# Kernel optimization log

Hardware: AMD Instinct MI355X
Metric: run time of the kernel (lower is better)

Reference implementation:

```python
import jax, jax.numpy as jnp
import numpy as np

B, T, IN, HID, LAT = 256, 512, 128, 64, 16

def _mk_lstm(key, in_dim, h_dim, scale):
    k1, k2, k3, k4 = jax.random.split(key, 4)
    return (jax.random.normal(k1, (4 * h_dim, in_dim), jnp.float32) * scale,
            jax.random.normal(k2, (4 * h_dim, h_dim), jnp.float32) * scale,
            jax.random.normal(k3, (4 * h_dim,), jnp.float32) * scale,
            jax.random.normal(k4, (4 * h_dim,), jnp.float32) * scale)

def setup_inputs() -> dict:
    key = jax.random.key(0)
    ks = jax.random.split(key, 5)
    x = jax.random.normal(ks[0], (B, T, IN), jnp.float32)
    out = {"x": x}
    dims = [(IN, HID, "e1"), (HID, LAT, "e2"), (LAT, HID, "d1"), (HID, IN, "d2")]
    for k, (di, dh, nm) in zip(ks[1:], dims):
        scale = 1.0 / np.sqrt(dh)  # pytorch LSTM init range ~ 1/sqrt(hidden)
        Wih, Whh, bih, bhh = _mk_lstm(k, di, dh, scale)
        out[f"Wih_{nm}"], out[f"Whh_{nm}"], out[f"bih_{nm}"], out[f"bhh_{nm}"] = Wih, Whh, bih, bhh
    return out

def lstm(x, Wih, Whh, bih, bhh):
    # x: [B,T,I]; gates ordered i,f,g,o as in torch.nn.LSTM
    H = Whh.shape[1]
    xg = jnp.einsum('bti,gi->btg', x, Wih) + bih + bhh  # [B,T,4H]
    def step(carry, xt):
        h, c = carry
        g = xt + h @ Whh.T
        i, f, gg, o = jnp.split(g, 4, axis=-1)
        c = jax.nn.sigmoid(f) * c + jax.nn.sigmoid(i) * jnp.tanh(gg)
        h = jax.nn.sigmoid(o) * jnp.tanh(c)
        return (h, c), h
    b = x.shape[0]
    h0 = jnp.zeros((b, H), x.dtype)
    _, hs = jax.lax.scan(step, (h0, h0), jnp.swapaxes(xg, 0, 1))
    return jnp.swapaxes(hs, 0, 1)  # [B,T,H]

def reference(x, Wih_e1, Whh_e1, bih_e1, bhh_e1, Wih_e2, Whh_e2, bih_e2, bhh_e2,
              Wih_d1, Whh_d1, bih_d1, bhh_d1, Wih_d2, Whh_d2, bih_d2, bhh_d2):
    # dropout layers are identity at inference
    out = jax.nn.relu(lstm(x, Wih_e1, Whh_e1, bih_e1, bhh_e1))
    out = jax.nn.relu(lstm(out, Wih_e2, Whh_e2, bih_e2, bhh_e2))
    latent = out[:, -1, :]                                  # [B,LAT]
    dec_in = jnp.broadcast_to(latent[:, None, :], (x.shape[0], x.shape[1], latent.shape[-1]))
    out = jax.nn.relu(lstm(dec_in, Wih_d1, Whh_d1, bih_d1, bhh_d1))
    return lstm(out, Wih_d2, Whh_d2, bih_d2, bhh_d2)        # [B,T,IN]
```

## Files before the change

kernel.cpp:

```cpp
#include <hip/hip_runtime.h>


#define BB 256
#define TT 512

typedef _Float16 half2v __attribute__((ext_vector_type(2)));

static __device__ __forceinline__ float dot2(half2v a, half2v b, float c){
  return __builtin_amdgcn_fdot2(a,b,c,false);
}
template<int CTRL>
static __device__ __forceinline__ float qb(float v){
  return __int_as_float(__builtin_amdgcn_update_dpp(0, __float_as_int(v), CTRL, 0xF, 0xF, true));
}
static __device__ __forceinline__ float qsum1(float v){ return v + qb<0xB1>(v); }
static __device__ __forceinline__ float qsum2(float v){ return v + qb<0x4E>(v); }
static __device__ __forceinline__ float hsum8(float v){
  v = qsum1(v); v = qsum2(v); return v + qb<0x141>(v);
}
static __device__ __forceinline__ float rcp_(float v){ return __builtin_amdgcn_rcpf(v); }
static __device__ __forceinline__ unsigned packh2(float lo, float hi){
  half2v p; p.x=(_Float16)lo; p.y=(_Float16)hi;
  return __builtin_bit_cast(unsigned, p);
}
static __device__ __forceinline__ half2v ash2(unsigned u){ return __builtin_bit_cast(half2v,u); }
static __device__ __forceinline__ half2v mkh2(float lo, float hi){
  half2v p; p.x=(_Float16)lo; p.y=(_Float16)hi; return p;
}

static __device__ __forceinline__ float lstm_update(int q, float a0, float a1,
                                                    float a2, float a3, float& c){
  float mine = a0;
  mine = (q==1) ? a1 : mine;
  mine = (q==2) ? a2 : mine;
  mine = (q==3) ? a3 : mine;
  const bool isg = (q==2);
  const float arg = isg ? (mine+mine) : mine;
  const float s   = rcp_(1.0f + __expf(-arg));
  const float act = isg ? (s+s-1.0f) : s;
  const float bi = qb<0x00>(act);
  const float bf = qb<0x55>(act);
  const float bg = qb<0xAA>(act);
  const float bo = qb<0xFF>(act);
  c = bf*c + bi*bg;
  const float s2 = rcp_(1.0f + __expf(-(c+c)));
  return bo*(s2+s2-1.0f);
}

__global__ void __launch_bounds__(512, 2) k_fused(
    const float* __restrict__ x,
    const float* __restrict__ WihE1, const float* __restrict__ WhhE1,
    const float* __restrict__ bihE1, const float* __restrict__ bhhE1,
    const float* __restrict__ WihE2, const float* __restrict__ WhhE2,
    const float* __restrict__ bihE2, const float* __restrict__ bhhE2,
    const float* __restrict__ WihD1, const float* __restrict__ WhhD1,
    const float* __restrict__ bihD1, const float* __restrict__ bhhD1,
    const float* __restrict__ WihD2, const float* __restrict__ WhhD2,
    const float* __restrict__ bihD2, const float* __restrict__ bhhD2,
    float* __restrict__ out)
{
  const int b = blockIdx.x, tid = threadIdx.x;

  __shared__ unsigned wD1L[8*1024];
  __shared__ unsigned vhE [2*96];
  __shared__ unsigned e2op[2*48];
  __shared__ unsigned dop [2*96];
  __shared__ unsigned vhD1[2*32];
  __shared__ float4   bD2L[128];
  __shared__ float4   pD1L[64];
  __shared__ float    latF[16];

  {
    const int o = tid & 7, j = tid >> 3;
    half2v w1[4][12];
    float bias1[4];
#pragma unroll
    for (int g=0; g<4; ++g){
      const int row = g*64 + j;
      bias1[g] = (o==0) ? (bihE1[row]+bhhE1[row]) : 0.0f;
#pragma unroll
      for (int m=0;m<12;++m){
        const int k0 = 24*o + 2*m;
        const float lo = (k0   < 128)? WihE1[row*128+k0]   : WhhE1[row*64 + (k0-128)];
        const float hi = (k0+1 < 128)? WihE1[row*128+k0+1] : WhhE1[row*64 + (k0+1-128)];
        w1[g][m] = mkh2(lo,hi);
      }
    }
    const bool e2act = (tid >= 64 && tid < 128);
    const int q2 = tid & 3, j2 = (tid - 64) >> 2;
    half2v w2[4][12];
    float bias2[4] = {0.f,0.f,0.f,0.f};
    if (e2act){
#pragma unroll
      for (int g=0; g<4; ++g){
        const int row = g*16 + j2;
        bias2[g] = (q2==0) ? (bihE2[row]+bhhE2[row]) : 0.0f;
#pragma unroll
        for (int m=0;m<12;++m){
          const int k0 = 24*q2 + 2*m;
          float lo = 0.0f, hi = 0.0f;
          if (k0 < 64)        lo = WihE2[row*64+k0];
          else if (k0 < 80)   lo = WhhE2[row*16 + (k0-64)];
          if (k0+1 < 64)      hi = WihE2[row*64+k0+1];
          else if (k0+1 < 80) hi = WhhE2[row*16 + (k0+1-64)];
          w2[g][m] = mkh2(lo,hi);
        }
      }
    }
    const bool xact = (tid < 64);
    const float* xrow = x + (size_t)b * (TT*128);
    float2 xa, xb;
    if (xact){
      float2 v0 = *(const float2*)(xrow + 2*tid);
      vhE[tid] = packh2(v0.x, v0.y);
      xa = *(const float2*)(xrow + 128 + 2*tid);
      xb = *(const float2*)(xrow + 256 + 2*tid);
    }
    if (tid >= 128 && tid < 160) vhE[64 + (tid-128)] = 0u;
    if (tid >= 160 && tid < 256) e2op[tid-160] = 0u;
    float c1 = 0.0f, c2 = 0.0f;
    __syncthreads();

#define XSTAGE(T, NXT) do{ if (xact){                                          \
      vhE[(NXT)*96 + tid] = packh2(xa.x, xa.y);                                \
      xa = xb;                                                                 \
      const int t3_ = ((T)+3 < TT) ? ((T)+3) : (TT-1);                         \
      xb = *(const float2*)(xrow + (size_t)t3_*128 + 2*tid);                   \
    } }while(0)

#define E1STEP(T, CUR) do{                                                     \
      float a0=bias1[0], a1=bias1[1], a2=bias1[2], a3=bias1[3];                \
      const uint4* vp = (const uint4*)(vhE + (CUR)*96 + o*12);                 \
      _Pragma("unroll")                                                        \
      for (int r=0;r<3;++r){                                                   \
        const uint4 u = vp[r];                                                 \
        const half2v o0=ash2(u.x), o1=ash2(u.y), o2=ash2(u.z), o3=ash2(u.w);   \
        a0=dot2(w1[0][4*r+0],o0,a0); a1=dot2(w1[1][4*r+0],o0,a1);              \
        a2=dot2(w1[2][4*r+0],o0,a2); a3=dot2(w1[3][4*r+0],o0,a3);              \
        a0=dot2(w1[0][4*r+1],o1,a0); a1=dot2(w1[1][4*r+1],o1,a1);              \
        a2=dot2(w1[2][4*r+1],o1,a2); a3=dot2(w1[3][4*r+1],o1,a3);              \
        a0=dot2(w1[0][4*r+2],o2,a0); a1=dot2(w1[1][4*r+2],o2,a1);              \
        a2=dot2(w1[2][4*r+2],o2,a2); a3=dot2(w1[3][4*r+2],o2,a3);              \
        a0=dot2(w1[0][4*r+3],o3,a0); a1=dot2(w1[1][4*r+3],o3,a1);              \
        a2=dot2(w1[2][4*r+3],o3,a2); a3=dot2(w1[3][4*r+3],o3,a3);              \
      }                                                                        \
      a0=hsum8(a0); a1=hsum8(a1); a2=hsum8(a2); a3=hsum8(a3);                  \
      const float h = lstm_update(o & 3, a0, a1, a2, a3, c1);                  \
      if (o == 0){                                                             \
        ((_Float16*)(vhE + ((CUR)^1)*96))[128 + j] = (_Float16)h;              \
        ((_Float16*)(e2op + (CUR)*48))[j]          = (_Float16)fmaxf(h, 0.0f); \
      }                                                                        \
    }while(0)

#define E2STEP(T2, CP) do{ if (e2act){                                         \
      float a0=bias2[0], a1=bias2[1], a2=bias2[2], a3=bias2[3];                \
      const uint4* vp = (const uint4*)(e2op + (CP)*48 + q2*12);                \
      _Pragma("unroll")                                                        \
      for (int r=0;r<3;++r){                                                   \
        const uint4 u = vp[r];                                                 \
        const half2v o0=ash2(u.x), o1=ash2(u.y), o2=ash2(u.z), o3=ash2(u.w);   \
        a0=dot2(w2[0][4*r+0],o0,a0); a1=dot2(w2[1][4*r+0],o0,a1);              \
        a2=dot2(w2[2][4*r+0],o0,a2); a3=dot2(w2[3][4*r+0],o0,a3);              \
        a0=dot2(w2[0][4*r+1],o1,a0); a1=dot2(w2[1][4*r+1],o1,a1);              \
        a2=dot2(w2[2][4*r+1],o1,a2); a3=dot2(w2[3][4*r+1],o1,a3);              \
        a0=dot2(w2[0][4*r+2],o2,a0); a1=dot2(w2[1][4*r+2],o2,a1);              \
        a2=dot2(w2[2][4*r+2],o2,a2); a3=dot2(w2[3][4*r+2],o2,a3);              \
        a0=dot2(w2[0][4*r+3],o3,a0); a1=dot2(w2[1][4*r+3],o3,a1);              \
        a2=dot2(w2[2][4*r+3],o3,a2); a3=dot2(w2[3][4*r+3],o3,a3);              \
      }                                                                        \
      a0=qsum2(qsum1(a0)); a1=qsum2(qsum1(a1));                                \
      a2=qsum2(qsum1(a2)); a3=qsum2(qsum1(a3));                                \
      const float h = lstm_update(q2, a0, a1, a2, a3, c2);                     \
      if (q2 == 0){                                                            \
        ((_Float16*)(e2op + ((CP)^1)*48))[64 + j2] = (_Float16)h;              \
        if ((T2) == TT-1) latF[j2] = fmaxf(h, 0.0f);                           \
      }                                                                        \
    } }while(0)

    XSTAGE(0, 1); E1STEP(0, 0);
    __syncthreads();
    for (int t = 1; t <= TT-3; t += 2){
      XSTAGE(t, 0);   E1STEP(t, 1);   E2STEP(t-1, 0);
      __syncthreads();
      XSTAGE(t+1, 1); E1STEP(t+1, 0); E2STEP(t, 1);
      __syncthreads();
    }
    XSTAGE(TT-1, 0); E1STEP(TT-1, 1); E2STEP(TT-2, 0);
    __syncthreads();
    E2STEP(TT-1, 1);
    __syncthreads();
#undef XSTAGE
#undef E1STEP
#undef E2STEP
  }
  __syncthreads();
  asm volatile("" ::: "memory");

  {
#pragma unroll
    for (int i=0;i<16;++i){
      const int idx = i*512 + tid;
      const int r = idx >> 10, rem = idx & 1023, l = rem >> 2, d = rem & 3;
      const int jd_ = l >> 2, qd_ = l & 3, g = r >> 1, m = ((r & 1) << 2) + d;
      const int row = g*64 + jd_, k0 = qd_*16 + 2*m;
      wD1L[idx] = packh2(WhhD1[row*64+k0], WhhD1[row*64+k0+1]);
    }
    if (tid < 128){
      float4 bb;
      bb.x = bihD2[0*128+tid] + bhhD2[0*128+tid];
      bb.y = bihD2[1*128+tid] + bhhD2[1*128+tid];
      bb.z = bihD2[2*128+tid] + bhhD2[2*128+tid];
      bb.w = bihD2[3*128+tid] + bhhD2[3*128+tid];
      bD2L[tid] = bb;
    }
    if (tid < 64){
      float4 pp;
#pragma unroll
      for (int g=0; g<4; ++g){
        const int row = g*64 + tid;
        float a = bihD1[row] + bhhD1[row];
#pragma unroll
        for (int i=0;i<16;++i) a = fmaf(WihD1[row*16+i], latF[i], a);
        (&pp.x)[g] = a;
      }
      pD1L[tid] = pp;
    }

    const int qd = tid & 3, jd = tid >> 2;
    half2v wD2[4][24];
#pragma unroll
    for (int g=0; g<4; ++g){
      const int row = g*128 + jd;
#pragma unroll
      for (int m=0;m<24;++m){
        const int k0 = 48*qd + 2*m;
        const float lo = (k0   < 64)? WihD2[row*64+k0]   : WhhD2[row*128+(k0-64)];
        const float hi = (k0+1 < 64)? WihD2[row*64+k0+1] : WhhD2[row*128+(k0+1-64)];
        wD2[g][m] = mkh2(lo,hi);
      }
    }
    const bool d1act = (tid < 256);
    if (tid < 64)                dop[32 + tid] = 0u;
    if (tid >= 64 && tid < 96)   vhD1[tid-64] = 0u;
    float cd1 = 0.0f, cd2 = 0.0f;
    float* orow = out + (size_t)b * (TT*128);
    __syncthreads();

#define D2STEP(T2, C2P) do{                                                    \
      float a0=0.f, a1=0.f, a2=0.f, a3=0.f;                                    \
      const uint4* vp = (const uint4*)(dop + (C2P)*96 + qd*24);                \
      _Pragma("unroll")                                                        \
      for (int r=0;r<6;++r){                                                   \
        const uint4 u = vp[r];                                                 \
        const half2v o0=ash2(u.x),o1=ash2(u.y),o2=ash2(u.z),o3=ash2(u.w);      \
        a0=dot2(wD2[0][4*r+0],o0,a0); a1=dot2(wD2[1][4*r+0],o0,a1);            \
        a2=dot2(wD2[2][4*r+0],o0,a2); a3=dot2(wD2[3][4*r+0],o0,a3);            \
        a0=dot2(wD2[0][4*r+1],o1,a0); a1=dot2(wD2[1][4*r+1],o1,a1);            \
        a2=dot2(wD2[2][4*r+1],o1,a2); a3=dot2(wD2[3][4*r+1],o1,a3);            \
        a0=dot2(wD2[0][4*r+2],o2,a0); a1=dot2(wD2[1][4*r+2],o2,a1);            \
        a2=dot2(wD2[2][4*r+2],o2,a2); a3=dot2(wD2[3][4*r+2],o2,a3);            \
        a0=dot2(wD2[0][4*r+3],o3,a0); a1=dot2(wD2[1][4*r+3],o3,a1);            \
        a2=dot2(wD2[2][4*r+3],o3,a2); a3=dot2(wD2[3][4*r+3],o3,a3);            \
      }                                                                        \
      a0=qsum2(qsum1(a0)); a1=qsum2(qsum1(a1));                                \
      a2=qsum2(qsum1(a2)); a3=qsum2(qsum1(a3));                                \
      const float4 bb = bD2L[jd];                                              \
      a0 += bb.x; a1 += bb.y; a2 += bb.z; a3 += bb.w;                          \
      const float h = lstm_update(qd, a0, a1, a2, a3, cd2);                    \
      if (qd==0){                                                              \
        ((_Float16*)(dop + ((C2P)^1)*96))[64 + jd] = (_Float16)h;              \
        orow[(size_t)(T2)*128 + jd] = h;                                       \
      }                                                                        \
    }while(0)

#define D1STEP(T, CUR) do{ if (d1act){                                         \
      const uint4* ov = (const uint4*)(vhD1 + (CUR)*32 + qd*8);                \
      const uint4 o01 = ov[0], o23 = ov[1];                                    \
      float a0=0.f, a1=0.f, a2=0.f, a3=0.f;                                    \
      {                                                                        \
        const uint4 wA = *(const uint4*)(wD1L + 0*1024 + tid*4);               \
        const uint4 wB = *(const uint4*)(wD1L + 1*1024 + tid*4);               \
        a0=dot2(ash2(wA.x),ash2(o01.x),a0); a0=dot2(ash2(wA.y),ash2(o01.y),a0);\
        a0=dot2(ash2(wA.z),ash2(o01.z),a0); a0=dot2(ash2(wA.w),ash2(o01.w),a0);\
        a0=dot2(ash2(wB.x),ash2(o23.x),a0); a0=dot2(ash2(wB.y),ash2(o23.y),a0);\
        a0=dot2(ash2(wB.z),ash2(o23.z),a0); a0=dot2(ash2(wB.w),ash2(o23.w),a0);\
      }                                                                        \
      {                                                                        \
        const uint4 wA = *(const uint4*)(wD1L + 2*1024 + tid*4);               \
        const uint4 wB = *(const uint4*)(wD1L + 3*1024 + tid*4);               \
        a1=dot2(ash2(wA.x),ash2(o01.x),a1); a1=dot2(ash2(wA.y),ash2(o01.y),a1);\
        a1=dot2(ash2(wA.z),ash2(o01.z),a1); a1=dot2(ash2(wA.w),ash2(o01.w),a1);\
        a1=dot2(ash2(wB.x),ash2(o23.x),a1); a1=dot2(ash2(wB.y),ash2(o23.y),a1);\
        a1=dot2(ash2(wB.z),ash2(o23.z),a1); a1=dot2(ash2(wB.w),ash2(o23.w),a1);\
      }                                                                        \
      {                                                                        \
        const uint4 wA = *(const uint4*)(wD1L + 4*1024 + tid*4);               \
        const uint4 wB = *(const uint4*)(wD1L + 5*1024 + tid*4);               \
        a2=dot2(ash2(wA.x),ash2(o01.x),a2); a2=dot2(ash2(wA.y),ash2(o01.y),a2);\
        a2=dot2(ash2(wA.z),ash2(o01.z),a2); a2=dot2(ash2(wA.w),ash2(o01.w),a2);\
        a2=dot2(ash2(wB.x),ash2(o23.x),a2); a2=dot2(ash2(wB.y),ash2(o23.y),a2);\
        a2=dot2(ash2(wB.z),ash2(o23.z),a2); a2=dot2(ash2(wB.w),ash2(o23.w),a2);\
      }                                                                        \
      {                                                                        \
        const uint4 wA = *(const uint4*)(wD1L + 6*1024 + tid*4);               \
        const uint4 wB = *(const uint4*)(wD1L + 7*1024 + tid*4);               \
        a3=dot2(ash2(wA.x),ash2(o01.x),a3); a3=dot2(ash2(wA.y),ash2(o01.y),a3);\
        a3=dot2(ash2(wA.z),ash2(o01.z),a3); a3=dot2(ash2(wA.w),ash2(o01.w),a3);\
        a3=dot2(ash2(wB.x),ash2(o23.x),a3); a3=dot2(ash2(wB.y),ash2(o23.y),a3);\
        a3=dot2(ash2(wB.z),ash2(o23.z),a3); a3=dot2(ash2(wB.w),ash2(o23.w),a3);\
      }                                                                        \
      a0=qsum2(qsum1(a0)); a1=qsum2(qsum1(a1));                                \
      a2=qsum2(qsum1(a2)); a3=qsum2(qsum1(a3));                                \
      const float4 pj = pD1L[jd];                                              \
      a0 += pj.x; a1 += pj.y; a2 += pj.z; a3 += pj.w;                          \
      const float h = lstm_update(qd, a0, a1, a2, a3, cd1);                    \
      if (qd==0){                                                              \
        ((_Float16*)(vhD1 + ((CUR)^1)*32))[jd] = (_Float16)h;                  \
        ((_Float16*)(dop + (CUR)*96))[jd]      = (_Float16)fmaxf(h,0.0f);      \
      }                                                                        \
    } }while(0)

    D1STEP(0, 0);
    __syncthreads();
    for (int t = 1; t <= TT-3; t += 2){
      D2STEP(t-1, 0); D1STEP(t, 1);
      __syncthreads();
      D2STEP(t, 1);   D1STEP(t+1, 0);
      __syncthreads();
    }
    D2STEP(TT-2, 0); D1STEP(TT-1, 1);
    __syncthreads();
    D2STEP(TT-1, 1);
#undef D2STEP
#undef D1STEP
  }
}

extern "C" void kernel_launch(void* const* d_in, const int* in_sizes, int n_in,
                              void* d_out, int out_size, void* d_ws, size_t ws_size,
                              hipStream_t stream) {
  const float* x      = (const float*)d_in[0];
  const float* WihE1  = (const float*)d_in[1];
  const float* WhhE1  = (const float*)d_in[2];
  const float* bihE1  = (const float*)d_in[3];
  const float* bhhE1  = (const float*)d_in[4];
  const float* WihE2  = (const float*)d_in[5];
  const float* WhhE2  = (const float*)d_in[6];
  const float* bihE2  = (const float*)d_in[7];
  const float* bhhE2  = (const float*)d_in[8];
  const float* WihD1  = (const float*)d_in[9];
  const float* WhhD1  = (const float*)d_in[10];
  const float* bihD1  = (const float*)d_in[11];
  const float* bhhD1  = (const float*)d_in[12];
  const float* WihD2  = (const float*)d_in[13];
  const float* WhhD2  = (const float*)d_in[14];
  const float* bihD2  = (const float*)d_in[15];
  const float* bhhD2  = (const float*)d_in[16];
  float* out = (float*)d_out;

  k_fused<<<BB, 512, 0, stream>>>(x,
      WihE1, WhhE1, bihE1, bhhE1,
      WihE2, WhhE2, bihE2, bhhE2,
      WihD1, WhhD1, bihD1, bhhD1,
      WihD2, WhhD2, bihD2, bhhD2,
      out);
}
```

Before: 775.4 us.

## Remap encoder warps: 4-lane E1 groups, E2 weights in LDS, separate x-stage warp

Encoder layer 1 now uses 4 lanes per hidden unit with 24 half2 weights per gate in registers, instead of 8 lanes with 12. This shortens the cross-lane reduction from three DPP steps to two. E2 weights move from registers into a shared-memory table read each step, and E1, E2 and the x staging are given separate waves (threads 0-255, 256-319, 320-383). The intent is to cut reduction latency on the serial critical path and avoid divergence inside one wave. In exchange, E1 register pressure roughly doubles, which risks spills under the 512-thread, 2-block launch bounds, and E2 pays extra LDS reads every step.

```diff
diff --git a/kernel.cpp b/kernel.cpp
--- a/kernel.cpp
+++ b/kernel.cpp
@@ -15,9 +15,6 @@
 }
 static __device__ __forceinline__ float qsum1(float v){ return v + qb<0xB1>(v); }
 static __device__ __forceinline__ float qsum2(float v){ return v + qb<0x4E>(v); }
-static __device__ __forceinline__ float hsum8(float v){
-  v = qsum1(v); v = qsum2(v); return v + qb<0x141>(v);
-}
 static __device__ __forceinline__ float rcp_(float v){ return __builtin_amdgcn_rcpf(v); }
 static __device__ __forceinline__ unsigned packh2(float lo, float hi){
   half2v p; p.x=(_Float16)lo; p.y=(_Float16)hi;
@@ -62,6 +59,7 @@
   const int b = blockIdx.x, tid = threadIdx.x;
 
   __shared__ unsigned wD1L[8*1024];
+  __shared__ unsigned e2wL[12*256];
   __shared__ unsigned vhE [2*96];
   __shared__ unsigned e2op[2*48];
   __shared__ unsigned dop [2*96];
@@ -71,50 +69,56 @@
   __shared__ float    latF[16];
 
   {
-    const int o = tid & 7, j = tid >> 3;
-    half2v w1[4][12];
-    float bias1[4];
-#pragma unroll
-    for (int g=0; g<4; ++g){
-      const int row = g*64 + j;
-      bias1[g] = (o==0) ? (bihE1[row]+bhhE1[row]) : 0.0f;
-#pragma unroll
-      for (int m=0;m<12;++m){
-        const int k0 = 24*o + 2*m;
-        const float lo = (k0   < 128)? WihE1[row*128+k0]   : WhhE1[row*64 + (k0-128)];
-        const float hi = (k0+1 < 128)? WihE1[row*128+k0+1] : WhhE1[row*64 + (k0+1-128)];
-        w1[g][m] = mkh2(lo,hi);
-      }
-    }
-    const bool e2act = (tid >= 64 && tid < 128);
-    const int q2 = tid & 3, j2 = (tid - 64) >> 2;
-    half2v w2[4][12];
-    float bias2[4] = {0.f,0.f,0.f,0.f};
-    if (e2act){
+#pragma unroll
+    for (int i=0;i<6;++i){
+      const int idx = i*512 + tid;
+      const int r_ = idx >> 8, rem = idx & 255, l = rem >> 2, d = rem & 3;
+      const int g = r_/3, rr = r_ - 3*g, m = rr*4 + d;
+      const int q2l = l & 3, j2l = l >> 2;
+      const int row = g*16 + j2l, k0 = q2l*24 + 2*m;
+      float lo = 0.0f, hi = 0.0f;
+      if (k0 < 64)        lo = WihE2[row*64+k0];
+      else if (k0 < 80)   lo = WhhE2[row*16 + (k0-64)];
+      if (k0+1 < 64)      hi = WihE2[row*64+k0+1];
+      else if (k0+1 < 80) hi = WhhE2[row*16 + (k0+1-64)];
+      e2wL[idx] = packh2(lo, hi);
+    }
+
+    const bool e1act = (tid < 256);
+    const int q = tid & 3, j = tid >> 2;
+    half2v w1[4][24];
+    float bias1[4] = {0.f,0.f,0.f,0.f};
+    if (e1act){
 #pragma unroll
       for (int g=0; g<4; ++g){
-        const int row = g*16 + j2;
-        bias2[g] = (q2==0) ? (bihE2[row]+bhhE2[row]) : 0.0f;
-#pragma unroll
-        for (int m=0;m<12;++m){
-          const int k0 = 24*q2 + 2*m;
-          float lo = 0.0f, hi = 0.0f;
-          if (k0 < 64)        lo = WihE2[row*64+k0];
-          else if (k0 < 80)   lo = WhhE2[row*16 + (k0-64)];
-          if (k0+1 < 64)      hi = WihE2[row*64+k0+1];
-          else if (k0+1 < 80) hi = WhhE2[row*16 + (k0+1-64)];
-          w2[g][m] = mkh2(lo,hi);
+        const int row = g*64 + j;
+        bias1[g] = (q==0) ? (bihE1[row]+bhhE1[row]) : 0.0f;
+#pragma unroll
+        for (int m=0;m<24;++m){
+          const int k0 = q*48 + 2*m;
+          const float lo = (k0   < 128)? WihE1[row*128+k0]   : WhhE1[row*64 + (k0-128)];
+          const float hi = (k0+1 < 128)? WihE1[row*128+k0+1] : WhhE1[row*64 + (k0+1-128)];
+          w1[g][m] = mkh2(lo,hi);
         }
       }
     }
-    const bool xact = (tid < 64);
+    const bool e2act = (tid >= 256 && tid < 320);
+    const int q2 = tid & 3, j2 = (tid & 63) >> 2;
+    const int l4 = (tid & 63) * 4;
+    float bias2[4] = {0.f,0.f,0.f,0.f};
+    if (e2act && q2 == 0){
+#pragma unroll
+      for (int g=0; g<4; ++g) bias2[g] = bihE2[g*16+j2] + bhhE2[g*16+j2];
+    }
+    const bool xact = (tid >= 320 && tid < 384);
+    const int  xl   = tid - 320;
     const float* xrow = x + (size_t)b * (TT*128);
     float2 xa, xb;
     if (xact){
-      float2 v0 = *(const float2*)(xrow + 2*tid);
-      vhE[tid] = packh2(v0.x, v0.y);
-      xa = *(const float2*)(xrow + 128 + 2*tid);
-      xb = *(const float2*)(xrow + 256 + 2*tid);
+      float2 v0 = *(const float2*)(xrow + 2*xl);
+      vhE[xl] = packh2(v0.x, v0.y);
+      xa = *(const float2*)(xrow + 128 + 2*xl);
+      xb = *(const float2*)(xrow + 256 + 2*xl);
     }
     if (tid >= 128 && tid < 160) vhE[64 + (tid-128)] = 0u;
     if (tid >= 160 && tid < 256) e2op[tid-160] = 0u;
@@ -122,17 +126,17 @@
     __syncthreads();
 
 #define XSTAGE(T, NXT) do{ if (xact){                                          \
-      vhE[(NXT)*96 + tid] = packh2(xa.x, xa.y);                                \
+      vhE[(NXT)*96 + xl] = packh2(xa.x, xa.y);                                 \
       xa = xb;                                                                 \
       const int t3_ = ((T)+3 < TT) ? ((T)+3) : (TT-1);                         \
-      xb = *(const float2*)(xrow + (size_t)t3_*128 + 2*tid);                   \
+      xb = *(const float2*)(xrow + (size_t)t3_*128 + 2*xl);                    \
     } }while(0)
 
-#define E1STEP(T, CUR) do{                                                     \
+#define E1STEP(T, CUR) do{ if (e1act){                                         \
       float a0=bias1[0], a1=bias1[1], a2=bias1[2], a3=bias1[3];                \
-      const uint4* vp = (const uint4*)(vhE + (CUR)*96 + o*12);                 \
+      const uint4* vp = (const uint4*)(vhE + (CUR)*96 + q*24);                 \
       _Pragma("unroll")                                                        \
-      for (int r=0;r<3;++r){                                                   \
+      for (int r=0;r<6;++r){                                                   \
         const uint4 u = vp[r];                                                 \
         const half2v o0=ash2(u.x), o1=ash2(u.y), o2=ash2(u.z), o3=ash2(u.w);   \
         a0=dot2(w1[0][4*r+0],o0,a0); a1=dot2(w1[1][4*r+0],o0,a1);              \
@@ -144,30 +148,35 @@
         a0=dot2(w1[0][4*r+3],o3,a0); a1=dot2(w1[1][4*r+3],o3,a1);              \
         a2=dot2(w1[2][4*r+3],o3,a2); a3=dot2(w1[3][4*r+3],o3,a3);              \
       }                                                                        \
-      a0=hsum8(a0); a1=hsum8(a1); a2=hsum8(a2); a3=hsum8(a3);                  \
-      const float h = lstm_update(o & 3, a0, a1, a2, a3, c1);                  \
-      if (o == 0){                                                             \
+      a0=qsum2(qsum1(a0)); a1=qsum2(qsum1(a1));                                \
+      a2=qsum2(qsum1(a2)); a3=qsum2(qsum1(a3));                                \
+      const float h = lstm_update(q, a0, a1, a2, a3, c1);                      \
+      if (q == 0){                                                             \
         ((_Float16*)(vhE + ((CUR)^1)*96))[128 + j] = (_Float16)h;              \
         ((_Float16*)(e2op + (CUR)*48))[j]          = (_Float16)fmaxf(h, 0.0f); \
       }                                                                        \
+    } }while(0)
+
+#define E2GATE(G, AG, U0, U1, U2) do{                                          \
+      const uint4 wA = *(const uint4*)(e2wL + ((G)*3+0)*256 + l4);             \
+      const uint4 wB = *(const uint4*)(e2wL + ((G)*3+1)*256 + l4);             \
+      const uint4 wC = *(const uint4*)(e2wL + ((G)*3+2)*256 + l4);             \
+      AG=dot2(ash2(wA.x),ash2(U0.x),AG); AG=dot2(ash2(wA.y),ash2(U0.y),AG);    \
+      AG=dot2(ash2(wA.z),ash2(U0.z),AG); AG=dot2(ash2(wA.w),ash2(U0.w),AG);    \
+      AG=dot2(ash2(wB.x),ash2(U1.x),AG); AG=dot2(ash2(wB.y),ash2(U1.y),AG);    \
+      AG=dot2(ash2(wB.z),ash2(U1.z),AG); AG=dot2(ash2(wB.w),ash2(U1.w),AG);    \
+      AG=dot2(ash2(wC.x),ash2(U2.x),AG); AG=dot2(ash2(wC.y),ash2(U2.y),AG);    \
+      AG=dot2(ash2(wC.z),ash2(U2.z),AG); AG=dot2(ash2(wC.w),ash2(U2.w),AG);    \
     }while(0)
 
 #define E2STEP(T2, CP) do{ if (e2act){                                         \
+      const uint4* ovp = (const uint4*)(e2op + (CP)*48 + q2*12);               \
+      const uint4 u0 = ovp[0], u1 = ovp[1], u2 = ovp[2];                       \
       float a0=bias2[0], a1=bias2[1], a2=bias2[2], a3=bias2[3];                \
-      const uint4* vp = (const uint4*)(e2op + (CP)*48 + q2*12);                \
-      _Pragma("unroll")                                                        \
-      for (int r=0;r<3;++r){                                                   \
-        const uint4 u = vp[r];                                                 \
-        const half2v o0=ash2(u.x), o1=ash2(u.y), o2=ash2(u.z), o3=ash2(u.w);   \
-        a0=dot2(w2[0][4*r+0],o0,a0); a1=dot2(w2[1][4*r+0],o0,a1);              \
-        a2=dot2(w2[2][4*r+0],o0,a2); a3=dot2(w2[3][4*r+0],o0,a3);              \
-        a0=dot2(w2[0][4*r+1],o1,a0); a1=dot2(w2[1][4*r+1],o1,a1);              \
-        a2=dot2(w2[2][4*r+1],o1,a2); a3=dot2(w2[3][4*r+1],o1,a3);              \
-        a0=dot2(w2[0][4*r+2],o2,a0); a1=dot2(w2[1][4*r+2],o2,a1);              \
-        a2=dot2(w2[2][4*r+2],o2,a2); a3=dot2(w2[3][4*r+2],o2,a3);              \
-        a0=dot2(w2[0][4*r+3],o3,a0); a1=dot2(w2[1][4*r+3],o3,a1);              \
-        a2=dot2(w2[2][4*r+3],o3,a2); a3=dot2(w2[3][4*r+3],o3,a3);              \
-      }                                                                        \
+      E2GATE(0, a0, u0, u1, u2);                                               \
+      E2GATE(1, a1, u0, u1, u2);                                               \
+      E2GATE(2, a2, u0, u1, u2);                                               \
+      E2GATE(3, a3, u0, u1, u2);                                               \
       a0=qsum2(qsum1(a0)); a1=qsum2(qsum1(a1));                                \
       a2=qsum2(qsum1(a2)); a3=qsum2(qsum1(a3));                                \
       const float h = lstm_update(q2, a0, a1, a2, a3, c2);                     \
@@ -191,6 +200,7 @@
     __syncthreads();
 #undef XSTAGE
 #undef E1STEP
+#undef E2GATE
 #undef E2STEP
   }
   __syncthreads();
```

Result: faster. 758.9 us (-2.1%).
